# Kernel tuning notes

Hardware: AMD Instinct MI355X
Metric: run time of the kernel (lower is better)

## Reference

```python
import jax, jax.numpy as jnp
import numpy as np

N = 262144   # total nodes
E = 1048576  # total edges
B = 512      # graphs per batch
IN, H, EDIM, AH, CH, NB = 8, 128, 4, 128, 128, 4

def _lin(key, fi, fo):
    # kaiming_normal fan_out/relu approximated with fan_in scaling (only affects init stats)
    return jax.random.normal(key, (fi, fo), jnp.float32) * np.sqrt(2.0 / fi)

def setup_inputs() -> dict:
    key = jax.random.key(0)
    ks = jax.random.split(key, 24)
    inp = {}
    inp['x'] = jax.random.normal(ks[0], (N, IN), jnp.float32)
    inp['edge_index'] = jax.random.randint(ks[1], (2, E), 0, N)
    inp['edge_attr'] = jax.random.normal(ks[2], (E, EDIM), jnp.float32)
    seg = N // B
    inp['batch'] = (jnp.arange(N) // seg).astype(jnp.int32)
    inp['ptr'] = (jnp.arange(B + 1) * seg).astype(jnp.int32)
    dims = [(IN, H), (H, H), (H, H)]  # final layer outputs embed_dim == H
    for l, (di, do) in enumerate(dims):
        inp[f'We{l}'] = _lin(ks[3 + 2 * l], EDIM, di)
        inp[f'be{l}'] = jnp.zeros((di,), jnp.float32)
        inp[f'W{l}'] = _lin(ks[4 + 2 * l], di, do)
        inp[f'b{l}'] = jnp.zeros((do,), jnp.float32)
    inp['laW1'] = _lin(ks[10], H, AH); inp['lab1'] = jnp.zeros((AH,), jnp.float32)
    inp['laW2'] = _lin(ks[11], AH, 1); inp['lab2'] = jnp.zeros((1,), jnp.float32)
    inp['maW1'] = _lin(ks[12], H, AH); inp['mab1'] = jnp.zeros((AH,), jnp.float32)
    inp['maW2'] = _lin(ks[13], AH, NB); inp['mab2'] = jnp.zeros((NB,), jnp.float32)
    inp['lcW1'] = _lin(ks[14], H, CH); inp['lcb1'] = jnp.zeros((CH,), jnp.float32)
    inp['lcW2'] = _lin(ks[15], CH, 1); inp['lcb2'] = jnp.zeros((1,), jnp.float32)
    inp['mcW1'] = _lin(ks[16], H, CH); inp['mcb1'] = jnp.zeros((CH,), jnp.float32)
    inp['mcW2'] = _lin(ks[17], CH, 1); inp['mcb2'] = jnp.zeros((1,), jnp.float32)
    return inp

def _gnn(x, edge_index, edge_attr, Wes, bes, Ws, bs):
    # GINE-style edge-conditioned message passing (dropout off / eval mode)
    src, dst = edge_index[0], edge_index[1]
    h = x
    for We, be, W, b in zip(Wes, bes, Ws, bs):
        msg = jax.nn.relu(h[src] + edge_attr @ We + be)            # [E, d]
        agg = jax.ops.segment_sum(msg, dst, num_segments=N)        # [N, d]
        h = jax.nn.relu((h + agg) @ W + b)
    return h

def reference(x, edge_index, edge_attr, batch, ptr,
              We0, be0, W0, b0, We1, be1, W1, b1, We2, be2, W2, b2,
              laW1, lab1, laW2, lab2, maW1, mab1, maW2, mab2,
              lcW1, lcb1, lcW2, lcb2, mcW1, mcb1, mcW2, mcb2):
    emb = _gnn(x, edge_index, edge_attr, [We0, We1, We2], [be0, be1, be2], [W0, W1, W2], [b0, b1, b2])  # [N, H]

    # per-node location logit, then fused segmented softmax over each graph's nodes
    loc_logits = (jax.nn.relu(emb @ laW1 + lab1) @ laW2 + lab2)[:, 0]  # [N]
    seg_max = jax.ops.segment_max(loc_logits, batch, num_segments=B)
    shifted = loc_logits - seg_max[batch]
    denom = jax.ops.segment_sum(jnp.exp(shifted), batch, num_segments=B)
    logp = shifted - jnp.log(denom)[batch]                              # per-node log-prob within its graph
    loc_entropy = -jax.ops.segment_sum(jnp.exp(logp) * logp, batch, num_segments=B)  # [B]

    # segmented categorical sampling via Gumbel-max (global node index, matching start+local_idx)
    key = jax.random.key(42)
    u = jax.random.uniform(key, (N,), minval=1e-6, maxval=1.0 - 1e-6)
    pert = loc_logits - jnp.log(-jnp.log(u))
    pmax = jax.ops.segment_max(pert, batch, num_segments=B)
    cand = jnp.where(pert >= pmax[batch], jnp.arange(N), N)
    locations = jax.ops.segment_min(cand, batch, num_segments=B)        # [B] global indices
    loc_log_probs = logp[locations]                                     # [B]

    sel = emb[locations]                                                # [B, H]
    mut_logits = jax.nn.relu(sel @ maW1 + mab1) @ maW2 + mab2           # [B, NB]
    mut_logp = jax.nn.log_softmax(mut_logits, axis=-1)
    mutations = jax.random.categorical(jax.random.fold_in(key, 1), mut_logits, axis=-1)  # [B]
    mut_log_probs = jnp.take_along_axis(mut_logp, mutations[:, None], axis=-1)[:, 0]
    mut_entropy = -jnp.sum(jnp.exp(mut_logp) * mut_logp, axis=-1)

    # critics: global_add_pool + MLP -> scalar per graph; mutation critic on selected node
    pooled = jax.ops.segment_sum(emb, batch, num_segments=B)            # [B, H]
    loc_values = (jax.nn.relu(pooled @ lcW1 + lcb1) @ lcW2 + lcb2)[:, 0]
    mut_values = (jax.nn.relu(sel @ mcW1 + mcb1) @ mcW2 + mcb2)[:, 0]

    return (locations, mutations, loc_log_probs, mut_log_probs,
            loc_entropy, mut_entropy, loc_values, mut_values, emb)
```

## Files before the change

kernel.cpp:

```cpp
#include <hip/hip_runtime.h>
#include <cstdint>
#include <cstddef>

#define NN 262144
#define EE 1048576
#define BB 512
#define SEG 512

__device__ __forceinline__ unsigned rotl32(unsigned x, int r) {
    return (x << r) | (x >> (32 - r));
}

__device__ __forceinline__ void tf2x32(unsigned k0, unsigned k1, unsigned x0, unsigned x1,
                                       unsigned& o0, unsigned& o1) {
    unsigned ks[3] = {k0, k1, k0 ^ k1 ^ 0x1BD11BDAu};
    x0 += ks[0]; x1 += ks[1];
    const int R0[4] = {13, 15, 26, 6};
    const int R1[4] = {17, 29, 16, 24};
#pragma unroll
    for (int i = 0; i < 5; ++i) {
        const int* R = (i & 1) ? R1 : R0;
#pragma unroll
        for (int j = 0; j < 4; ++j) {
            x0 += x1;
            x1 = rotl32(x1, R[j]);
            x1 ^= x0;
        }
        x0 += ks[(i + 1) % 3];
        x1 += ks[(i + 2) % 3] + (unsigned)(i + 1);
    }
    o0 = x0; o1 = x1;
}

__device__ __forceinline__ float unif_loc(unsigned idx) {
    unsigned j = idx & (NN / 2 - 1);
    unsigned half = idx >> 17;
    unsigned o0, o1;
    tf2x32(0u, 42u, j, j + (unsigned)(NN / 2), o0, o1);
    unsigned bits = half ? o1 : o0;
    float f = __uint_as_float((bits >> 9) | 0x3F800000u) - 1.0f;
    const float minv = 1e-6f;
    const float maxv = 1.0f - 1e-6f;
    const float span = maxv - minv;
    return fmaxf(minv, __fadd_rn(__fmul_rn(f, span), minv));
}

__global__ void csr_count(const int* __restrict__ dst, int* __restrict__ counts, int E) {
    int i = blockIdx.x * 256 + threadIdx.x;
    if (i < E) atomicAdd(&counts[dst[i]], 1);
}

__global__ void scan512(const int* __restrict__ in, int* __restrict__ outExcl, int* __restrict__ bsum) {
    __shared__ int s[512];
    int b = blockIdx.x, tid = threadIdx.x;
    int v = in[(size_t)b * 512 + tid];
    s[tid] = v;
    __syncthreads();
    for (int d = 1; d < 512; d <<= 1) {
        int add = (tid >= d) ? s[tid - d] : 0;
        __syncthreads();
        s[tid] += add;
        __syncthreads();
    }
    outExcl[(size_t)b * 512 + tid] = s[tid] - v;
    if (tid == 511) bsum[b] = s[511];
}

__global__ void scan_fix(int* __restrict__ offs, const int* __restrict__ bbase,
                         int* __restrict__ cursor, int N, int E) {
    int gid = blockIdx.x * 512 + threadIdx.x;
    int v = offs[gid] + bbase[blockIdx.x];
    offs[gid] = v;
    cursor[gid] = v;
    if (gid == 0) offs[N] = E;
}

__global__ void csr_fill(const int* __restrict__ dst, const int* __restrict__ src,
                         const float4* __restrict__ ea, int* __restrict__ cursor,
                         int* __restrict__ ssrc, float4* __restrict__ sea, int E) {
    int i = blockIdx.x * 256 + threadIdx.x;
    if (i < E) {
        int p = atomicAdd(&cursor[dst[i]], 1);
        ssrc[p] = src[i];
        sea[p] = ea[i];
    }
}

__global__ void agg_l0(const float* __restrict__ x, const int* __restrict__ ssrc,
                       const float4* __restrict__ sea, const int* __restrict__ offs,
                       const float* __restrict__ We0, const float* __restrict__ be0,
                       float* __restrict__ out) {
    __shared__ float Ws[32];
    __shared__ float bs[8];
    int tid = threadIdx.x;
    if (tid < 32) Ws[tid] = We0[tid];
    if (tid < 8) bs[tid] = be0[tid];
    __syncthreads();
    int n = blockIdx.x * 256 + tid;
    float a[8] = {0.f, 0.f, 0.f, 0.f, 0.f, 0.f, 0.f, 0.f};
    int pb = offs[n], pe = offs[n + 1];
    for (int p = pb; p < pe; ++p) {
        int s = ssrc[p];
        float4 ev = sea[p];
        float4 xa = *(const float4*)(x + (size_t)s * 8);
        float4 xb = *(const float4*)(x + (size_t)s * 8 + 4);
        float xs[8] = {xa.x, xa.y, xa.z, xa.w, xb.x, xb.y, xb.z, xb.w};
#pragma unroll
        for (int j2 = 0; j2 < 8; ++j2) {
            float m = xs[j2] + bs[j2] + ev.x * Ws[j2] + ev.y * Ws[8 + j2] +
                      ev.z * Ws[16 + j2] + ev.w * Ws[24 + j2];
            a[j2] += fmaxf(m, 0.f);
        }
    }
    float4 o0 = {a[0], a[1], a[2], a[3]};
    float4 o1 = {a[4], a[5], a[6], a[7]};
    *(float4*)(out + (size_t)n * 8) = o0;
    *(float4*)(out + (size_t)n * 8 + 4) = o1;
}

__global__ void update_l0(const float* __restrict__ x, const float* __restrict__ agg0,
                          const float* __restrict__ W0, const float* __restrict__ b0,
                          float* __restrict__ h1) {
    __shared__ float Ws[8 * 128];
    __shared__ float bs[128];
    __shared__ float ts[2][8];
    int tid = threadIdx.x;
#pragma unroll
    for (int i = tid; i < 1024; i += 256) Ws[i] = W0[i];
    if (tid < 128) bs[tid] = b0[tid];
    int sub = tid >> 7;
    int c = tid & 127;
    int node = blockIdx.x * 2 + sub;
    if (c < 8) ts[sub][c] = x[(size_t)node * 8 + c] + agg0[(size_t)node * 8 + c];
    __syncthreads();
    float acc = bs[c];
#pragma unroll
    for (int k = 0; k < 8; ++k) acc = fmaf(ts[sub][k], Ws[k * 128 + c], acc);
    h1[(size_t)node * 128 + c] = fmaxf(acc, 0.f);
}

#define MSG(hv, ev)                                                                 \
    {                                                                               \
        float mx = hv.x + bv.x + ev.x * w0.x + ev.y * w1.x + ev.z * w2.x + ev.w * w3.x; \
        float my = hv.y + bv.y + ev.x * w0.y + ev.y * w1.y + ev.z * w2.y + ev.w * w3.y; \
        acc.x += fmaxf(mx, 0.f);                                                    \
        acc.y += fmaxf(my, 0.f);                                                    \
    }

__global__ __launch_bounds__(256) void agg_l(const float2* __restrict__ h2,
                                             const int* __restrict__ ssrc,
                                             const float4* __restrict__ sea,
                                             const int* __restrict__ offs,
                                             const float* __restrict__ We,
                                             const float* __restrict__ be,
                                             float2* __restrict__ out) {
    int tid = threadIdx.x;
    int node = blockIdx.x * 4 + (tid >> 6);
    node = __builtin_amdgcn_readfirstlane(node);
    int lane = tid & 63;
    const float2* We2 = (const float2*)We;
    float2 w0 = We2[lane], w1 = We2[64 + lane], w2 = We2[128 + lane], w3 = We2[192 + lane];
    float2 bv = ((const float2*)be)[lane];
    float2 acc; acc.x = 0.f; acc.y = 0.f;
    int pb = offs[node], pe = offs[node + 1];
    int p = pb;
    for (; p + 4 <= pe; p += 4) {
        int s0 = ssrc[p], s1 = ssrc[p + 1], s2 = ssrc[p + 2], s3 = ssrc[p + 3];
        float4 e0 = sea[p], e1 = sea[p + 1], e2 = sea[p + 2], e3 = sea[p + 3];
        float2 ha = h2[(size_t)s0 * 64 + lane];
        float2 hb = h2[(size_t)s1 * 64 + lane];
        float2 hc = h2[(size_t)s2 * 64 + lane];
        float2 hd = h2[(size_t)s3 * 64 + lane];
        MSG(ha, e0) MSG(hb, e1) MSG(hc, e2) MSG(hd, e3)
    }
    for (; p < pe; ++p) {
        int s0 = ssrc[p];
        float4 e0 = sea[p];
        float2 ha = h2[(size_t)s0 * 64 + lane];
        MSG(ha, e0)
    }
    out[(size_t)node * 64 + lane] = acc;
}


typedef __attribute__((ext_vector_type(8))) short bf16x8;
typedef __attribute__((ext_vector_type(4))) float f32x4;

__device__ __forceinline__ ushort bf16r(float x) {
    unsigned u = __float_as_uint(x);
    return (ushort)((u + 0x7FFFu + ((u >> 16) & 1u)) >> 16);
}
__device__ __forceinline__ float bf2f(ushort h) {
    return __uint_as_float(((unsigned)h) << 16);
}

__global__ void pack3(const float* __restrict__ W1, const float* __restrict__ W2,
                      const float* __restrict__ LA, uint4* __restrict__ dst) {
    const float* W = (blockIdx.x == 0) ? W1 : (blockIdx.x == 1) ? W2 : LA;
    uint4* ph = dst + (size_t)blockIdx.x * 4096;
    uint4* pl = ph + 2048;
    int t = threadIdx.x;
    int l = t & 63, q = t >> 6;
    int lo = l & 15, kg = l >> 4;
    for (int i = 0; i < 8; ++i) {
        int combo = q * 8 + i;
        int kc = combo >> 3, n = combo & 7;
        ushort h8[8], l8[8];
#pragma unroll
        for (int j = 0; j < 8; ++j) {
            float wv = W[(size_t)(kc * 32 + kg * 8 + j) * 128 + n * 16 + lo];
            ushort hh = bf16r(wv);
            h8[j] = hh;
            l8[j] = bf16r(wv - bf2f(hh));
        }
        int idx = (kc * 8 + n) * 64 + l;
        ph[idx] = *(const uint4*)h8;
        pl[idx] = *(const uint4*)l8;
    }
}

__device__ __forceinline__ void load_a_frags(const float* P, const float* Q, int r0,
                                             int lo, int kg, int kc,
                                             bf16x8& ah0, bf16x8& al0,
                                             bf16x8& ah1, bf16x8& al1) {
#pragma unroll
    for (int m = 0; m < 2; ++m) {
        const float* ap = P + (size_t)(r0 + m * 16 + lo) * 128 + kc * 32 + kg * 8;
        float4 p0 = *(const float4*)ap;
        float4 p1 = *(const float4*)(ap + 4);
        if (Q) {
            const float* qp = Q + (size_t)(r0 + m * 16 + lo) * 128 + kc * 32 + kg * 8;
            float4 q0 = *(const float4*)qp;
            float4 q1 = *(const float4*)(qp + 4);
            p0.x += q0.x; p0.y += q0.y; p0.z += q0.z; p0.w += q0.w;
            p1.x += q1.x; p1.y += q1.y; p1.z += q1.z; p1.w += q1.w;
        }
        float av[8] = {p0.x, p0.y, p0.z, p0.w, p1.x, p1.y, p1.z, p1.w};
        bf16x8 ah, al;
#pragma unroll
        for (int j = 0; j < 8; ++j) {
            ushort hh = bf16r(av[j]);
            ah[j] = (short)hh;
            al[j] = (short)bf16r(av[j] - bf2f(hh));
        }
        if (m == 0) { ah0 = ah; al0 = al; } else { ah1 = ah; al1 = al; }
    }
}

__global__ __launch_bounds__(256) void gemm_mfma(const float* __restrict__ P, const float* Q,
                                                 const uint4* __restrict__ Wh,
                                                 const uint4* __restrict__ Wl,
                                                 const float* __restrict__ bias,
                                                 float* out) {
    int tid = threadIdx.x;
    int w = tid >> 6, l = tid & 63;
    int r0 = blockIdx.x * 128 + w * 32;
    int lo = l & 15, kg = l >> 4;
    const bf16x8* Bh = (const bf16x8*)Wh;
    const bf16x8* Bl = (const bf16x8*)Wl;
    f32x4 acc[2][8];
#pragma unroll
    for (int m = 0; m < 2; ++m)
#pragma unroll
        for (int n = 0; n < 8; ++n) acc[m][n] = (f32x4){0.f, 0.f, 0.f, 0.f};

    for (int kc = 0; kc < 4; ++kc) {
        bf16x8 ah0, al0, ah1, al1;
        load_a_frags(P, Q, r0, lo, kg, kc, ah0, al0, ah1, al1);
#pragma unroll
        for (int h2i = 0; h2i < 2; ++h2i) {
            bf16x8 bh[4], bl[4];
#pragma unroll
            for (int nn = 0; nn < 4; ++nn) {
                int idx = (kc * 8 + h2i * 4 + nn) * 64 + l;
                bh[nn] = Bh[idx];
                bl[nn] = Bl[idx];
            }
#pragma unroll
            for (int nn = 0; nn < 4; ++nn) {
                int n = h2i * 4 + nn;
                acc[0][n] = __builtin_amdgcn_mfma_f32_16x16x32_bf16(ah0, bh[nn], acc[0][n], 0, 0, 0);
                acc[0][n] = __builtin_amdgcn_mfma_f32_16x16x32_bf16(al0, bh[nn], acc[0][n], 0, 0, 0);
                acc[0][n] = __builtin_amdgcn_mfma_f32_16x16x32_bf16(ah0, bl[nn], acc[0][n], 0, 0, 0);
                acc[1][n] = __builtin_amdgcn_mfma_f32_16x16x32_bf16(ah1, bh[nn], acc[1][n], 0, 0, 0);
                acc[1][n] = __builtin_amdgcn_mfma_f32_16x16x32_bf16(al1, bh[nn], acc[1][n], 0, 0, 0);
                acc[1][n] = __builtin_amdgcn_mfma_f32_16x16x32_bf16(ah1, bl[nn], acc[1][n], 0, 0, 0);
            }
        }
    }
    float bv[8];
#pragma unroll
    for (int n = 0; n < 8; ++n) bv[n] = bias[n * 16 + lo];
#pragma unroll
    for (int m = 0; m < 2; ++m)
#pragma unroll
        for (int n = 0; n < 8; ++n)
#pragma unroll
            for (int v = 0; v < 4; ++v) {
                size_t g = (size_t)(r0 + m * 16 + kg * 4 + v) * 128 + n * 16 + lo;
                out[g] = fmaxf(acc[m][n][v] + bv[n], 0.f);
            }
}

__global__ __launch_bounds__(256) void gemm_logit_mfma(const float* __restrict__ P,
                                                       const uint4* __restrict__ Wh,
                                                       const uint4* __restrict__ Wl,
                                                       const float* __restrict__ bias,
                                                       const float* __restrict__ w2,
                                                       const float* __restrict__ b2,
                                                       float* __restrict__ L) {
    int tid = threadIdx.x;
    int w = tid >> 6, l = tid & 63;
    int r0 = blockIdx.x * 128 + w * 32;
    int lo = l & 15, kg = l >> 4;
    const bf16x8* Bh = (const bf16x8*)Wh;
    const bf16x8* Bl = (const bf16x8*)Wl;
    f32x4 acc[2][8];
#pragma unroll
    for (int m = 0; m < 2; ++m)
#pragma unroll
        for (int n = 0; n < 8; ++n) acc[m][n] = (f32x4){0.f, 0.f, 0.f, 0.f};

    for (int kc = 0; kc < 4; ++kc) {
        bf16x8 ah0, al0, ah1, al1;
        load_a_frags(P, (const float*)0, r0, lo, kg, kc, ah0, al0, ah1, al1);
#pragma unroll
        for (int h2i = 0; h2i < 2; ++h2i) {
            bf16x8 bh[4], bl[4];
#pragma unroll
            for (int nn = 0; nn < 4; ++nn) {
                int idx = (kc * 8 + h2i * 4 + nn) * 64 + l;
                bh[nn] = Bh[idx];
                bl[nn] = Bl[idx];
            }
#pragma unroll
            for (int nn = 0; nn < 4; ++nn) {
                int n = h2i * 4 + nn;
                acc[0][n] = __builtin_amdgcn_mfma_f32_16x16x32_bf16(ah0, bh[nn], acc[0][n], 0, 0, 0);
                acc[0][n] = __builtin_amdgcn_mfma_f32_16x16x32_bf16(al0, bh[nn], acc[0][n], 0, 0, 0);
                acc[0][n] = __builtin_amdgcn_mfma_f32_16x16x32_bf16(ah0, bl[nn], acc[0][n], 0, 0, 0);
                acc[1][n] = __builtin_amdgcn_mfma_f32_16x16x32_bf16(ah1, bh[nn], acc[1][n], 0, 0, 0);
                acc[1][n] = __builtin_amdgcn_mfma_f32_16x16x32_bf16(al1, bh[nn], acc[1][n], 0, 0, 0);
                acc[1][n] = __builtin_amdgcn_mfma_f32_16x16x32_bf16(ah1, bl[nn], acc[1][n], 0, 0, 0);
            }
        }
    }
    float bv[8], w2v[8];
#pragma unroll
    for (int n = 0; n < 8; ++n) {
        bv[n] = bias[n * 16 + lo];
        w2v[n] = w2[n * 16 + lo];
    }
    float b2v = b2[0];
#pragma unroll
    for (int m = 0; m < 2; ++m)
#pragma unroll
        for (int v = 0; v < 4; ++v) {
            float s = 0.f;
#pragma unroll
            for (int n = 0; n < 8; ++n)
                s += fmaxf(acc[m][n][v] + bv[n], 0.f) * w2v[n];
            s += __shfl_xor(s, 8);
            s += __shfl_xor(s, 4);
            s += __shfl_xor(s, 2);
            s += __shfl_xor(s, 1);
            if (lo == 0) L[r0 + m * 16 + kg * 4 + v] = s + b2v;
        }
}

__global__ void sample_k(const float* __restrict__ L, float* __restrict__ ob,
                         int* __restrict__ locInt) {
    int g = blockIdx.x, tid = threadIdx.x;
    __shared__ float sh[512];
    __shared__ float rb[256];
    __shared__ int ib[256];
    float l0 = L[g * 512 + tid];
    float l1 = L[g * 512 + 256 + tid];
    rb[tid] = fmaxf(l0, l1);
    __syncthreads();
    for (int s2 = 128; s2 > 0; s2 >>= 1) {
        if (tid < s2) rb[tid] = fmaxf(rb[tid], rb[tid + s2]);
        __syncthreads();
    }
    float mx = rb[0];
    __syncthreads();
    float s0 = l0 - mx, s1 = l1 - mx;
    sh[tid] = s0; sh[256 + tid] = s1;
    float e0 = expf(s0), e1 = expf(s1);
    rb[tid] = e0 + e1;
    __syncthreads();
    for (int s2 = 128; s2 > 0; s2 >>= 1) {
        if (tid < s2) rb[tid] += rb[tid + s2];
        __syncthreads();
    }
    float denom = rb[0];
    __syncthreads();
    rb[tid] = e0 * s0 + e1 * s1;
    __syncthreads();
    for (int s2 = 128; s2 > 0; s2 >>= 1) {
        if (tid < s2) rb[tid] += rb[tid + s2];
        __syncthreads();
    }
    float sum2 = rb[0];
    __syncthreads();
    unsigned i0 = (unsigned)(g * 512 + tid);
    unsigned i1 = i0 + 256u;
    float p0 = l0 - logf(-logf(unif_loc(i0)));
    float p1 = l1 - logf(-logf(unif_loc(i1)));
    rb[tid] = fmaxf(p0, p1);
    __syncthreads();
    for (int s2 = 128; s2 > 0; s2 >>= 1) {
        if (tid < s2) rb[tid] = fmaxf(rb[tid], rb[tid + s2]);
        __syncthreads();
    }
    float pmax = rb[0];
    __syncthreads();
    int c0 = (p0 >= pmax) ? tid : 0x7FFFFFFF;
    int c1 = (p1 >= pmax) ? (tid + 256) : 0x7FFFFFFF;
    ib[tid] = min(c0, c1);
    __syncthreads();
    for (int s2 = 128; s2 > 0; s2 >>= 1) {
        if (tid < s2) ib[tid] = min(ib[tid], ib[tid + s2]);
        __syncthreads();
    }
    if (tid == 0) {
        int li = ib[0];
        float logD = logf(denom);
        ob[g] = (float)(g * 512 + li);
        ob[1024 + g] = sh[li] - logD;
        ob[2048 + g] = logD - sum2 / denom;
        locInt[g] = g * 512 + li;
    }
}

__global__ void pool_k(const float* __restrict__ emb, float* __restrict__ pooled) {
    int g = blockIdx.x, tid = threadIdx.x;
    int c = tid & 127, rg = tid >> 7;
    __shared__ float sh[512];
    float s0 = 0.f, s1 = 0.f, s2 = 0.f, s3 = 0.f;
    const float* base = emb + ((size_t)g * 512 + (size_t)rg * 128) * 128 + c;
    for (int n = 0; n < 128; n += 4) {
        s0 += base[(size_t)(n + 0) * 128];
        s1 += base[(size_t)(n + 1) * 128];
        s2 += base[(size_t)(n + 2) * 128];
        s3 += base[(size_t)(n + 3) * 128];
    }
    sh[tid] = (s0 + s1) + (s2 + s3);
    __syncthreads();
    if (rg == 0) pooled[g * 128 + c] = sh[c] + sh[128 + c] + sh[256 + c] + sh[384 + c];
}

__global__ void heads_k(const float* __restrict__ emb, const float* __restrict__ pooled,
                        const int* __restrict__ locInt,
                        const float* __restrict__ maW1, const float* __restrict__ mab1,
                        const float* __restrict__ maW2, const float* __restrict__ mab2,
                        const float* __restrict__ lcW1, const float* __restrict__ lcb1,
                        const float* __restrict__ lcW2, const float* __restrict__ lcb2,
                        const float* __restrict__ mcW1, const float* __restrict__ mcb1,
                        const float* __restrict__ mcW2, const float* __restrict__ mcb2,
                        float* __restrict__ ob) {
    int g = blockIdx.x, tid = threadIdx.x;
    __shared__ float sel[128], pl[128];
    __shared__ float red[4][128];
    __shared__ float red1[128];
    __shared__ float mcv_sh;
    sel[tid] = emb[(size_t)locInt[g] * 128 + tid];
    pl[tid] = pooled[g * 128 + tid];
    __syncthreads();
    float h = mab1[tid];
    for (int k = 0; k < 128; ++k) h = fmaf(sel[k], maW1[k * 128 + tid], h);
    h = fmaxf(h, 0.f);
    red[0][tid] = h * maW2[tid * 4 + 0];
    red[1][tid] = h * maW2[tid * 4 + 1];
    red[2][tid] = h * maW2[tid * 4 + 2];
    red[3][tid] = h * maW2[tid * 4 + 3];
    __syncthreads();
    for (int s2 = 64; s2 > 0; s2 >>= 1) {
        if (tid < s2) {
            red[0][tid] += red[0][tid + s2];
            red[1][tid] += red[1][tid + s2];
            red[2][tid] += red[2][tid + s2];
            red[3][tid] += red[3][tid + s2];
        }
        __syncthreads();
    }
    float h2 = mcb1[tid];
    for (int k = 0; k < 128; ++k) h2 = fmaf(sel[k], mcW1[k * 128 + tid], h2);
    h2 = fmaxf(h2, 0.f);
    red1[tid] = h2 * mcW2[tid];
    __syncthreads();
    for (int s2 = 64; s2 > 0; s2 >>= 1) {
        if (tid < s2) red1[tid] += red1[tid + s2];
        __syncthreads();
    }
    if (tid == 0) mcv_sh = red1[0] + mcb2[0];
    __syncthreads();
    float h3 = lcb1[tid];
    for (int k = 0; k < 128; ++k) h3 = fmaf(pl[k], lcW1[k * 128 + tid], h3);
    h3 = fmaxf(h3, 0.f);
    red1[tid] = h3 * lcW2[tid];
    __syncthreads();
    for (int s2 = 64; s2 > 0; s2 >>= 1) {
        if (tid < s2) red1[tid] += red1[tid + s2];
        __syncthreads();
    }
    if (tid == 0) {
        float lcv = red1[0] + lcb2[0];
        float lg[4];
#pragma unroll
        for (int c = 0; c < 4; ++c) lg[c] = red[c][0] + mab2[c];
        unsigned fk0, fk1;
        tf2x32(0u, 42u, 0u, 1u, fk0, fk1);
        float gmb[4];
#pragma unroll
        for (int c = 0; c < 4; ++c) {
            unsigned m = (unsigned)(g * 4 + c);
            unsigned j = m & 1023u;
            unsigned halfb = m >> 10;
            unsigned o0, o1;
            tf2x32(fk0, fk1, j, j + 1024u, o0, o1);
            unsigned bits = halfb ? o1 : o0;
            float f = __uint_as_float((bits >> 9) | 0x3F800000u) - 1.0f;
            const float tiny = 1.17549435e-38f;
            float u = fmaxf(tiny, __fadd_rn(__fmul_rn(f, 1.0f), tiny));
            gmb[c] = -logf(-logf(u));
        }
        int best = 0;
        float bz = gmb[0] + lg[0];
#pragma unroll
        for (int c = 1; c < 4; ++c) {
            float z = gmb[c] + lg[c];
            if (z > bz) { bz = z; best = c; }
        }
        float M = fmaxf(fmaxf(lg[0], lg[1]), fmaxf(lg[2], lg[3]));
        float se = 0.f;
#pragma unroll
        for (int c = 0; c < 4; ++c) se += expf(lg[c] - M);
        float lse = M + logf(se);
        float ent = 0.f;
#pragma unroll
        for (int c = 0; c < 4; ++c) {
            float lp = lg[c] - lse;
            ent -= expf(lp) * lp;
        }
        ob[512 + g] = (float)best;
        ob[1536 + g] = lg[best] - lse;
        ob[2560 + g] = ent;
        ob[3072 + g] = lcv;
        ob[3584 + g] = mcv_sh;
    }
}

extern "C" void kernel_launch(void* const* d_in, const int* in_sizes, int n_in,
                              void* d_out, int out_size, void* d_ws, size_t ws_size,
                              hipStream_t stream) {
    const float* x   = (const float*)d_in[0];
    const int* ei    = (const int*)d_in[1];
    const float* ea  = (const float*)d_in[2];
    const float* We0 = (const float*)d_in[5];
    const float* be0 = (const float*)d_in[6];
    const float* W0  = (const float*)d_in[7];
    const float* b0  = (const float*)d_in[8];
    const float* We1 = (const float*)d_in[9];
    const float* be1 = (const float*)d_in[10];
    const float* W1  = (const float*)d_in[11];
    const float* b1  = (const float*)d_in[12];
    const float* We2 = (const float*)d_in[13];
    const float* be2 = (const float*)d_in[14];
    const float* W2  = (const float*)d_in[15];
    const float* b2  = (const float*)d_in[16];
    const float* laW1 = (const float*)d_in[17];
    const float* lab1 = (const float*)d_in[18];
    const float* laW2 = (const float*)d_in[19];
    const float* lab2 = (const float*)d_in[20];
    const float* maW1 = (const float*)d_in[21];
    const float* mab1 = (const float*)d_in[22];
    const float* maW2 = (const float*)d_in[23];
    const float* mab2 = (const float*)d_in[24];
    const float* lcW1 = (const float*)d_in[25];
    const float* lcb1 = (const float*)d_in[26];
    const float* lcW2 = (const float*)d_in[27];
    const float* lcb2 = (const float*)d_in[28];
    const float* mcW1 = (const float*)d_in[29];
    const float* mcb1 = (const float*)d_in[30];
    const float* mcW2 = (const float*)d_in[31];
    const float* mcb2 = (const float*)d_in[32];

    float* out = (float*)d_out;
    char* ws = (char*)d_ws;
    size_t off = 0;
    auto alloc = [&](size_t bytes) -> void* {
        void* p = ws + off;
        off += (bytes + 255) & ~(size_t)255;
        return p;
    };
    float* U    = (float*)alloc((size_t)NN * 128 * 4);
    int* counts = (int*)alloc((size_t)NN * 4);
    int* offs   = (int*)alloc((size_t)(NN + 1) * 4);
    int* cursor = (int*)alloc((size_t)NN * 4);
    int* ssrc   = (int*)alloc((size_t)EE * 4);
    float4* sea = (float4*)alloc((size_t)EE * 16);
    int* bsum   = (int*)alloc(512 * 4);
    int* bbase  = (int*)alloc(512 * 4);
    int* bscr   = (int*)alloc(512 * 4);
    float* Lg   = (float*)alloc((size_t)NN * 4);
    float* pooled = (float*)alloc((size_t)BB * 128 * 4);
    int* locInt = (int*)alloc((size_t)BB * 4);

    const int* src = ei;
    const int* dstA = ei + EE;
    float* V = out + 4096;
    float* agg0 = U;

    uint4* wpack = (uint4*)cursor;

    hipMemsetAsync(counts, 0, (size_t)NN * 4, stream);
    csr_count<<<EE / 256, 256, 0, stream>>>(dstA, counts, EE);
    scan512<<<NN / 512, 512, 0, stream>>>(counts, offs, bsum);
    scan512<<<1, 512, 0, stream>>>(bsum, bbase, bscr);
    scan_fix<<<NN / 512, 512, 0, stream>>>(offs, bbase, cursor, NN, EE);
    csr_fill<<<EE / 256, 256, 0, stream>>>(dstA, src, (const float4*)ea, cursor, ssrc, sea, EE);
    pack3<<<3, 256, 0, stream>>>(W1, W2, laW1, wpack);

    agg_l0<<<NN / 256, 256, 0, stream>>>(x, ssrc, sea, offs, We0, be0, agg0);
    update_l0<<<NN / 2, 256, 0, stream>>>(x, agg0, W0, b0, V);
    agg_l<<<NN / 4, 256, 0, stream>>>((const float2*)V, ssrc, sea, offs, We1, be1, (float2*)U);
    gemm_mfma<<<NN / 128, 256, 0, stream>>>(V, U, wpack, wpack + 2048, b1, U);
    agg_l<<<NN / 4, 256, 0, stream>>>((const float2*)U, ssrc, sea, offs, We2, be2, (float2*)V);
    gemm_mfma<<<NN / 128, 256, 0, stream>>>(U, V, wpack + 4096, wpack + 6144, b2, V);

    gemm_logit_mfma<<<NN / 128, 256, 0, stream>>>(V, wpack + 8192, wpack + 10240, lab1, laW2, lab2, Lg);
    sample_k<<<BB, 256, 0, stream>>>(Lg, out, locInt);

    pool_k<<<BB, 512, 0, stream>>>(V, pooled);
    heads_k<<<BB, 128, 0, stream>>>(V, pooled, locInt, maW1, mab1, maW2, mab2,
                                    lcW1, lcb1, lcW2, lcb2, mcW1, mcb1, mcW2, mcb2, out);
}
```

Baseline: 927.3 us.

## Process four consecutive destination nodes per wavefront in edge aggregation

The layer-1/2 aggregation kernel now gives each 64-lane wavefront four consecutive destination nodes and walks their combined CSR edge range as one stream. Each edge's message goes to one of four accumulators, selected by comparing the edge position with the node offsets. The loop is unrolled 8-wide so more independent gathers are in flight. This targets the short per-node loops (about 4 edges on average) and their remainder overhead, at the cost of extra select arithmetic per edge and more registers.

Measured after the change: 907.2 us. -2.2%, faster.

```diff
diff --git a/kernel.cpp b/kernel.cpp
--- a/kernel.cpp
+++ b/kernel.cpp
@@ -139,14 +139,6 @@
     h1[(size_t)node * 128 + c] = fmaxf(acc, 0.f);
 }
 
-#define MSG(hv, ev)                                                                 \
-    {                                                                               \
-        float mx = hv.x + bv.x + ev.x * w0.x + ev.y * w1.x + ev.z * w2.x + ev.w * w3.x; \
-        float my = hv.y + bv.y + ev.x * w0.y + ev.y * w1.y + ev.z * w2.y + ev.w * w3.y; \
-        acc.x += fmaxf(mx, 0.f);                                                    \
-        acc.y += fmaxf(my, 0.f);                                                    \
-    }
-
 __global__ __launch_bounds__(256) void agg_l(const float2* __restrict__ h2,
                                              const int* __restrict__ ssrc,
                                              const float4* __restrict__ sea,
@@ -155,31 +147,70 @@
                                              const float* __restrict__ be,
                                              float2* __restrict__ out) {
     int tid = threadIdx.x;
-    int node = blockIdx.x * 4 + (tid >> 6);
-    node = __builtin_amdgcn_readfirstlane(node);
     int lane = tid & 63;
+    int n0 = blockIdx.x * 16 + (tid >> 6) * 4;
+    n0 = __builtin_amdgcn_readfirstlane(n0);
     const float2* We2 = (const float2*)We;
     float2 w0 = We2[lane], w1 = We2[64 + lane], w2 = We2[128 + lane], w3 = We2[192 + lane];
     float2 bv = ((const float2*)be)[lane];
-    float2 acc; acc.x = 0.f; acc.y = 0.f;
-    int pb = offs[node], pe = offs[node + 1];
-    int p = pb;
-    for (; p + 4 <= pe; p += 4) {
-        int s0 = ssrc[p], s1 = ssrc[p + 1], s2 = ssrc[p + 2], s3 = ssrc[p + 3];
-        float4 e0 = sea[p], e1 = sea[p + 1], e2 = sea[p + 2], e3 = sea[p + 3];
-        float2 ha = h2[(size_t)s0 * 64 + lane];
-        float2 hb = h2[(size_t)s1 * 64 + lane];
-        float2 hc = h2[(size_t)s2 * 64 + lane];
-        float2 hd = h2[(size_t)s3 * 64 + lane];
-        MSG(ha, e0) MSG(hb, e1) MSG(hc, e2) MSG(hd, e3)
-    }
-    for (; p < pe; ++p) {
+    float2 a0 = {0.f, 0.f}, a1 = {0.f, 0.f}, a2 = {0.f, 0.f}, a3 = {0.f, 0.f};
+
+    int4 ov = *(const int4*)(offs + n0);
+    int o0 = ov.x, o1 = ov.y, o2 = ov.z, o3 = ov.w;
+    int o4 = offs[n0 + 4];
+
+#define ACCSEL(hv, ev, pp)                                                              \
+    {                                                                                   \
+        float mx = hv.x + bv.x + ev.x * w0.x + ev.y * w1.x + ev.z * w2.x + ev.w * w3.x; \
+        float my = hv.y + bv.y + ev.x * w0.y + ev.y * w1.y + ev.z * w2.y + ev.w * w3.y; \
+        mx = fmaxf(mx, 0.f);                                                            \
+        my = fmaxf(my, 0.f);                                                            \
+        int id = (int)((pp) >= o1) + (int)((pp) >= o2) + (int)((pp) >= o3);             \
+        a0.x += (id == 0) ? mx : 0.f; a0.y += (id == 0) ? my : 0.f;                     \
+        a1.x += (id == 1) ? mx : 0.f; a1.y += (id == 1) ? my : 0.f;                     \
+        a2.x += (id == 2) ? mx : 0.f; a2.y += (id == 2) ? my : 0.f;                     \
+        a3.x += (id == 3) ? mx : 0.f; a3.y += (id == 3) ? my : 0.f;                     \
+    }
+
+    int p = o0;
+    for (; p + 8 <= o4; p += 8) {
+        int s_[8];
+#pragma unroll
+        for (int j = 0; j < 8; ++j) s_[j] = ssrc[p + j];
+        float4 e_[8];
+#pragma unroll
+        for (int j = 0; j < 8; ++j) e_[j] = sea[p + j];
+        float2 h_[8];
+#pragma unroll
+        for (int j = 0; j < 8; ++j) h_[j] = h2[(size_t)s_[j] * 64 + lane];
+#pragma unroll
+        for (int j = 0; j < 8; ++j) ACCSEL(h_[j], e_[j], p + j)
+    }
+    for (; p + 4 <= o4; p += 4) {
+        int s_[4];
+#pragma unroll
+        for (int j = 0; j < 4; ++j) s_[j] = ssrc[p + j];
+        float4 e_[4];
+#pragma unroll
+        for (int j = 0; j < 4; ++j) e_[j] = sea[p + j];
+        float2 h_[4];
+#pragma unroll
+        for (int j = 0; j < 4; ++j) h_[j] = h2[(size_t)s_[j] * 64 + lane];
+#pragma unroll
+        for (int j = 0; j < 4; ++j) ACCSEL(h_[j], e_[j], p + j)
+    }
+    for (; p < o4; ++p) {
         int s0 = ssrc[p];
         float4 e0 = sea[p];
         float2 ha = h2[(size_t)s0 * 64 + lane];
-        MSG(ha, e0)
-    }
-    out[(size_t)node * 64 + lane] = acc;
+        ACCSEL(ha, e0, p)
+    }
+#undef ACCSEL
+
+    out[(size_t)(n0 + 0) * 64 + lane] = a0;
+    out[(size_t)(n0 + 1) * 64 + lane] = a1;
+    out[(size_t)(n0 + 2) * 64 + lane] = a2;
+    out[(size_t)(n0 + 3) * 64 + lane] = a3;
 }
 
 
@@ -624,9 +655,9 @@
 
     agg_l0<<<NN / 256, 256, 0, stream>>>(x, ssrc, sea, offs, We0, be0, agg0);
     update_l0<<<NN / 2, 256, 0, stream>>>(x, agg0, W0, b0, V);
-    agg_l<<<NN / 4, 256, 0, stream>>>((const float2*)V, ssrc, sea, offs, We1, be1, (float2*)U);
+    agg_l<<<NN / 16, 256, 0, stream>>>((const float2*)V, ssrc, sea, offs, We1, be1, (float2*)U);
     gemm_mfma<<<NN / 128, 256, 0, stream>>>(V, U, wpack, wpack + 2048, b1, U);
-    agg_l<<<NN / 4, 256, 0, stream>>>((const float2*)U, ssrc, sea, offs, We2, be2, (float2*)V);
+    agg_l<<<NN / 16, 256, 0, stream>>>((const float2*)U, ssrc, sea, offs, We2, be2, (float2*)V);
     gemm_mfma<<<NN / 128, 256, 0, stream>>>(U, V, wpack + 4096, wpack + 6144, b2, V);
 
     gemm_logit_mfma<<<NN / 128, 256, 0, stream>>>(V, wpack + 8192, wpack + 10240, lab1, laW2, lab2, Lg);
```

## Process eight destination nodes per wave in edge aggregation with flush-on-boundary

Applied to the files above, without the earlier changes.

The layer-1/2 aggregation kernel now assigns eight consecutive destination nodes to each wavefront. It walks their combined CSR edge range in batches of eight, with the eight gathers issued together, and writes each node's accumulator when the edge index crosses that node's boundary. This is meant to raise memory-level parallelism and cut per-node loop overhead and load imbalance from short adjacency lists. The cost is a data-dependent flush loop inside the inner loop, more registers, and one eighth as many blocks.

Result: faster. 908.8 us (-2.0%).

```diff
diff --git a/kernel.cpp b/kernel.cpp
--- a/kernel.cpp
+++ b/kernel.cpp
@@ -139,14 +139,6 @@
     h1[(size_t)node * 128 + c] = fmaxf(acc, 0.f);
 }
 
-#define MSG(hv, ev)                                                                 \
-    {                                                                               \
-        float mx = hv.x + bv.x + ev.x * w0.x + ev.y * w1.x + ev.z * w2.x + ev.w * w3.x; \
-        float my = hv.y + bv.y + ev.x * w0.y + ev.y * w1.y + ev.z * w2.y + ev.w * w3.y; \
-        acc.x += fmaxf(mx, 0.f);                                                    \
-        acc.y += fmaxf(my, 0.f);                                                    \
-    }
-
 __global__ __launch_bounds__(256) void agg_l(const float2* __restrict__ h2,
                                              const int* __restrict__ ssrc,
                                              const float4* __restrict__ sea,
@@ -155,31 +147,71 @@
                                              const float* __restrict__ be,
                                              float2* __restrict__ out) {
     int tid = threadIdx.x;
-    int node = blockIdx.x * 4 + (tid >> 6);
-    node = __builtin_amdgcn_readfirstlane(node);
     int lane = tid & 63;
+    int n0 = blockIdx.x * 32 + (tid >> 6) * 8;
+    n0 = __builtin_amdgcn_readfirstlane(n0);
     const float2* We2 = (const float2*)We;
     float2 w0 = We2[lane], w1 = We2[64 + lane], w2 = We2[128 + lane], w3 = We2[192 + lane];
     float2 bv = ((const float2*)be)[lane];
-    float2 acc; acc.x = 0.f; acc.y = 0.f;
-    int pb = offs[node], pe = offs[node + 1];
-    int p = pb;
-    for (; p + 4 <= pe; p += 4) {
-        int s0 = ssrc[p], s1 = ssrc[p + 1], s2 = ssrc[p + 2], s3 = ssrc[p + 3];
-        float4 e0 = sea[p], e1 = sea[p + 1], e2 = sea[p + 2], e3 = sea[p + 3];
-        float2 ha = h2[(size_t)s0 * 64 + lane];
-        float2 hb = h2[(size_t)s1 * 64 + lane];
-        float2 hc = h2[(size_t)s2 * 64 + lane];
-        float2 hd = h2[(size_t)s3 * 64 + lane];
-        MSG(ha, e0) MSG(hb, e1) MSG(hc, e2) MSG(hd, e3)
-    }
-    for (; p < pe; ++p) {
+
+    int b0  = __builtin_amdgcn_readfirstlane(offs[n0 + 0]);
+    int nb0 = __builtin_amdgcn_readfirstlane(offs[n0 + 1]);
+    int nb1 = __builtin_amdgcn_readfirstlane(offs[n0 + 2]);
+    int nb2 = __builtin_amdgcn_readfirstlane(offs[n0 + 3]);
+    int nb3 = __builtin_amdgcn_readfirstlane(offs[n0 + 4]);
+    int nb4 = __builtin_amdgcn_readfirstlane(offs[n0 + 5]);
+    int nb5 = __builtin_amdgcn_readfirstlane(offs[n0 + 6]);
+    int nb6 = __builtin_amdgcn_readfirstlane(offs[n0 + 7]);
+    int nb7 = __builtin_amdgcn_readfirstlane(offs[n0 + 8]);
+    int pend = nb7;
+
+    float2 acc = {0.f, 0.f};
+    float2* optr = out + (size_t)n0 * 64 + lane;
+
+#define FLUSH(pp)                                        \
+    while ((pp) == nb0) {                                \
+        *optr = acc;                                     \
+        acc.x = 0.f; acc.y = 0.f;                        \
+        optr += 64;                                      \
+        nb0 = nb1; nb1 = nb2; nb2 = nb3; nb3 = nb4;      \
+        nb4 = nb5; nb5 = nb6; nb6 = nb7; nb7 = 0x7FFFFFFF; \
+    }
+
+#define ACC(hv, ev)                                                                     \
+    {                                                                                   \
+        float mx = hv.x + bv.x + ev.x * w0.x + ev.y * w1.x + ev.z * w2.x + ev.w * w3.x; \
+        float my = hv.y + bv.y + ev.x * w0.y + ev.y * w1.y + ev.z * w2.y + ev.w * w3.y; \
+        acc.x += fmaxf(mx, 0.f);                                                        \
+        acc.y += fmaxf(my, 0.f);                                                        \
+    }
+
+    int p = b0;
+    for (; p + 8 <= pend; p += 8) {
+        int s_[8];
+#pragma unroll
+        for (int j = 0; j < 8; ++j) s_[j] = ssrc[p + j];
+        float4 e_[8];
+#pragma unroll
+        for (int j = 0; j < 8; ++j) e_[j] = sea[p + j];
+        float2 h_[8];
+#pragma unroll
+        for (int j = 0; j < 8; ++j) h_[j] = h2[(size_t)s_[j] * 64 + lane];
+#pragma unroll
+        for (int j = 0; j < 8; ++j) {
+            FLUSH(p + j)
+            ACC(h_[j], e_[j])
+        }
+    }
+    for (; p < pend; ++p) {
+        FLUSH(p)
         int s0 = ssrc[p];
         float4 e0 = sea[p];
         float2 ha = h2[(size_t)s0 * 64 + lane];
-        MSG(ha, e0)
-    }
-    out[(size_t)node * 64 + lane] = acc;
+        ACC(ha, e0)
+    }
+    FLUSH(pend)
+#undef ACC
+#undef FLUSH
 }
 
 
@@ -624,9 +656,9 @@
 
     agg_l0<<<NN / 256, 256, 0, stream>>>(x, ssrc, sea, offs, We0, be0, agg0);
     update_l0<<<NN / 2, 256, 0, stream>>>(x, agg0, W0, b0, V);
-    agg_l<<<NN / 4, 256, 0, stream>>>((const float2*)V, ssrc, sea, offs, We1, be1, (float2*)U);
+    agg_l<<<NN / 32, 256, 0, stream>>>((const float2*)V, ssrc, sea, offs, We1, be1, (float2*)U);
     gemm_mfma<<<NN / 128, 256, 0, stream>>>(V, U, wpack, wpack + 2048, b1, U);
-    agg_l<<<NN / 4, 256, 0, stream>>>((const float2*)U, ssrc, sea, offs, We2, be2, (float2*)V);
+    agg_l<<<NN / 32, 256, 0, stream>>>((const float2*)U, ssrc, sea, offs, We2, be2, (float2*)V);
     gemm_mfma<<<NN / 128, 256, 0, stream>>>(U, V, wpack + 4096, wpack + 6144, b2, V);
 
     gemm_logit_mfma<<<NN / 128, 256, 0, stream>>>(V, wpack + 8192, wpack + 10240, lab1, laW2, lab2, Lg);
```
